# Kernel tuning notes

Hardware: AMD Instinct MI355X
Metric: run time of the kernel (lower is better)

The kernel has to match this reference:

```python
import jax, jax.numpy as jnp
import numpy as np

NEG_SLOPE = 0.2

def _lrelu(x):
    return jax.nn.leaky_relu(x, NEG_SLOPE)

def _seg_mean(vals, seg_ids, num_segments):
    # scatter-mean: sum per segment / count (count clamped to 1 -> zeros for empty nodes,
    # matching torch version where untouched nodes keep new_x == 0)
    s = jax.ops.segment_sum(vals, seg_ids, num_segments=num_segments)
    c = jax.ops.segment_sum(jnp.ones((vals.shape[0], 1), vals.dtype), seg_ids, num_segments=num_segments)
    return s / jnp.maximum(c, 1.0)

def _messages(x, src, dst, rel, ts, rel_emb, time_emb, W_rt, b_rt, W_fc, b_fc):
    # MessagePassing.forward: rel_e = lrelu(rel_t_trans(cat(rel_e, time_e)));
    # m = lrelu(fc(cat(x[src], rel_e, x[dst])))
    rel_e = _lrelu(jnp.concatenate([rel_emb[rel], time_emb[ts]], axis=-1) @ W_rt + b_rt)  # [E, 2h]
    m = _lrelu(jnp.concatenate([x[src], rel_e, x[dst]], axis=-1) @ W_fc + b_fc)           # [E, 2h]
    return m

def setup_inputs() -> dict:
    key = jax.random.key(0)
    ks = jax.random.split(key, 16)
    N, F, H, E, B = 20000, 128, 64, 200000, 256
    NUM_REL, NUM_TS, MAX_ENT = 200, 365, 5000
    s = 0.05
    inp = {}
    inp['x_feat'] = jax.random.normal(ks[0], (N, F), jnp.float32)
    inp['node_grp_emb'] = jax.random.normal(ks[1], (MAX_ENT, H), jnp.float32) * s
    inp['rel_emb'] = jax.random.normal(ks[2], (NUM_REL, H), jnp.float32) * s
    # TimeEncode (TGAT-style fixed frequencies): cos(t * 1/10^(linspace(0,9,H)))
    t = jnp.arange(NUM_TS, dtype=jnp.float32)
    freq = 1.0 / (10.0 ** jnp.linspace(0.0, 9.0, H, dtype=jnp.float32))
    inp['time_emb'] = jnp.cos(t[:, None] * freq[None, :])
    inp['W_node'] = jax.random.normal(ks[3], (F, H), jnp.float32) * s
    inp['b_node'] = jnp.zeros((H,), jnp.float32)
    inp['W_rt'] = jax.random.normal(ks[4], (2 * H, 2 * H), jnp.float32) * s
    inp['b_rt'] = jnp.zeros((2 * H,), jnp.float32)
    inp['W_fc'] = jax.random.normal(ks[5], (6 * H, 2 * H), jnp.float32) * s
    inp['b_fc'] = jnp.zeros((2 * H,), jnp.float32)
    inp['w_pred'] = jax.random.normal(ks[6], (6 * H, 1), jnp.float32) * s
    inp['b_pred'] = jnp.zeros((1,), jnp.float32)
    inp['node_ent'] = jax.random.randint(ks[7], (N,), 0, MAX_ENT)
    inp['edge_src'] = jax.random.randint(ks[8], (E,), 0, N)
    inp['edge_dst'] = jax.random.randint(ks[9], (E,), 0, N)
    inp['edge_type'] = jax.random.randint(ks[10], (E,), 0, NUM_REL)
    inp['edge_ts'] = jax.random.randint(ks[11], (E,), 0, NUM_TS)
    inp['q_s'] = jax.random.randint(ks[12], (B,), 0, N)
    inp['q_o'] = jax.random.randint(ks[13], (B,), 0, N)
    inp['q_r'] = jax.random.randint(ks[14], (B,), 0, NUM_REL)
    inp['q_t'] = jax.random.randint(ks[15], (B,), 0, NUM_TS)
    inp['num_hops'] = 2
    return inp

def reference(x_feat, node_grp_emb, rel_emb, time_emb, W_node, b_node, W_rt, b_rt,
              W_fc, b_fc, w_pred, b_pred, node_ent, edge_src, edge_dst, edge_type,
              edge_ts, q_s, q_o, q_r, q_t, num_hops):
    N = x_feat.shape[0]
    # node init: x = cat(lrelu(node_emb(feat)), node_grp_emb[ent])  (dropout = eval identity)
    x = jnp.concatenate([_lrelu(x_feat @ W_node + b_node), node_grp_emb[node_ent]], axis=-1)  # [N, 2h]
    # multi-hop gather -> edge MLP -> scatter-mean (frontier loop flattened to num_hops full passes)
    for _ in range(num_hops):
        m = _messages(x, edge_src, edge_dst, edge_type, edge_ts, rel_emb, time_emb, W_rt, b_rt, W_fc, b_fc)
        x = x + _seg_mean(m, edge_dst, N)
    # final aggregation only into query destination nodes q_o
    m = _messages(x, edge_src, edge_dst, edge_type, edge_ts, rel_emb, time_emb, W_rt, b_rt, W_fc, b_fc)
    agg = _seg_mean(m, edge_dst, N)
    qo_mask = jnp.zeros((N, 1), x.dtype).at[q_o].set(1.0)
    x = x + agg * qo_mask
    # query relation/time transform and prediction
    q_r_t = _lrelu(jnp.concatenate([rel_emb[q_r], time_emb[q_t]], axis=-1) @ W_rt + b_rt)  # [B, 2h]
    final_feat = jnp.concatenate([x[q_s], q_r_t, x[q_o]], axis=-1)                          # [B, 6h]
    out = jax.nn.sigmoid(final_feat @ w_pred + b_pred)
    return out.squeeze(-1)
```

## Files before the change

### kernel.cpp

```cpp
#include <hip/hip_runtime.h>
#include <cstddef>
#include <cstdint>

#define H 64
#define TWOH 128
#define CAP 96
#define LRELU(v) ((v) >= 0.f ? (v) : 0.2f * (v))

typedef __attribute__((ext_vector_type(4))) float f32x4;
typedef __attribute__((ext_vector_type(8))) short bf16x8;

__device__ inline unsigned short f2bf(float f) {
    union { float f; unsigned u; } v; v.f = f;
    unsigned u = v.u + 0x7FFFu + ((v.u >> 16) & 1u);
    return (unsigned short)(u >> 16);
}
__device__ inline float bf2f(unsigned u16) {
    union { unsigned u; float f; } v; v.u = u16 << 16; return v.f;
}

__global__ __launch_bounds__(256) void k_setup(
    const float* __restrict__ xf, const float* __restrict__ grp,
    const float* __restrict__ Wn, const float* __restrict__ bn,
    const int* __restrict__ ent, float* __restrict__ x, unsigned short* __restrict__ xb,
    const float* __restrict__ Wfc, unsigned short* __restrict__ WT,
    const float* __restrict__ rel_emb, const float* __restrict__ time_emb,
    const float* __restrict__ Wrt, const float* __restrict__ brt,
    const int* __restrict__ qr, const int* __restrict__ qt,
    float* __restrict__ AR, float* __restrict__ BT, float* __restrict__ qrt,
    const int* __restrict__ src, const int* __restrict__ dst,
    const int* __restrict__ etype, const int* __restrict__ ets,
    int* deg, int2* __restrict__ a_sc,
    int N, int E, int B, int NUM_REL, int NUM_TS,
    int NB_NI, int NB_TW, int NB_RT)
{
    int b = blockIdx.x, t = threadIdx.x;
    __shared__ float s_u[32][128];
    if (b < NB_NI) {
        int n0 = b * 32;
        int w = t >> 6, l = t & 63;
#pragma unroll
        for (int i = 0; i < 4; ++i) {
            int idx = t + i * 256; int r = idx >> 5, c4 = (idx & 31) * 4;
            int n = n0 + r;
            float4 v = make_float4(0.f, 0.f, 0.f, 0.f);
            if (n < N) v = *(const float4*)(xf + (size_t)n * 128 + c4);
            *(float4*)(&s_u[r][c4]) = v;
        }
        __syncthreads();
        float acc[8];
#pragma unroll
        for (int r = 0; r < 8; ++r) acc[r] = 0.f;
        for (int k = 0; k < 128; ++k) {
            float wv = Wn[k * H + l];
#pragma unroll
            for (int r = 0; r < 8; ++r) acc[r] += s_u[w * 8 + r][k] * wv;
        }
        float bb = bn[l];
        for (int r = 0; r < 8; ++r) {
            int n = n0 + w * 8 + r; if (n >= N) break;
            float v = LRELU(acc[r] + bb);
            float g = grp[(size_t)ent[n] * H + l];
            x[(size_t)n * TWOH + l]      = v;
            x[(size_t)n * TWOH + H + l]  = g;
            xb[(size_t)n * TWOH + l]     = f2bf(v);
            xb[(size_t)n * TWOH + H + l] = f2bf(g);
        }
    } else if (b < NB_NI + NB_TW) {
        int tid = (b - NB_NI) * 256 + t;
        int m = tid >> 14, rem = tid & 16383, col = rem >> 7, k = rem & 127;
        WT[(size_t)m * 16384 + col * 128 + k] = f2bf(Wfc[((size_t)m * 128 + k) * 128 + col]);
    } else if (b < NB_NI + NB_TW + NB_RT) {
        int sub = t >> 7, tt = t & 127;
        int row = (b - NB_NI - NB_TW) * 2 + sub;
        int RT_ROWS = NUM_REL + NUM_TS + B;
        int valid = row < RT_ROWS;
        int type = 0, ridx = 0;
        if (valid) {
            if (row < NUM_REL)               { type = 0; ridx = row; }
            else if (row < NUM_REL + NUM_TS) { type = 1; ridx = row - NUM_REL; }
            else                             { type = 2; ridx = row - NUM_REL - NUM_TS; }
        }
        float lv = 0.f;
        if (valid) {
            if (type == 0)      lv = (tt < H) ? rel_emb[(size_t)ridx * H + tt] : 0.f;
            else if (type == 1) lv = (tt >= H) ? time_emb[(size_t)ridx * H + (tt - H)] : 0.f;
            else                lv = (tt < H) ? rel_emb[(size_t)qr[ridx] * H + tt]
                                              : time_emb[(size_t)qt[ridx] * H + (tt - H)];
        }
        s_u[sub][tt] = lv;
        __syncthreads();
        if (valid) {
            float acc = 0.f;
            for (int k = 0; k < 128; ++k) acc += s_u[sub][k] * Wrt[(size_t)k * TWOH + tt];
            if (type != 1) acc += brt[tt];
            if (type == 2) acc = LRELU(acc);
            if (type == 0)      AR[(size_t)ridx * TWOH + tt]  = acc;
            else if (type == 1) BT[(size_t)ridx * TWOH + tt]  = acc;
            else                qrt[(size_t)ridx * TWOH + tt] = acc;
        }
    } else {
        int e = (b - NB_NI - NB_TW - NB_RT) * 256 + t;
        if (e < E) {
            int dn = dst[e];
            int pos = atomicAdd(&deg[dn], 1);
            a_sc[(size_t)dn * CAP + pos] = make_int2(src[e], etype[e] * NUM_TS + ets[e]);
        }
    }
}

__global__ __launch_bounds__(256) void k_mid3(
    const float* __restrict__ AR, const float* __restrict__ BT,
    const unsigned short* __restrict__ WT, const float* __restrict__ bd,
    unsigned short* __restrict__ RE2b, int NC, int NUM_TS,
    const unsigned short* __restrict__ xb,
    unsigned short* __restrict__ XSb, unsigned short* __restrict__ XDb, int N,
    const int* __restrict__ qo, int* maski, int* __restrict__ qlist, int* cntQ, int B,
    int NB_RE2, int NB_G)
{
    __shared__ __align__(16) char smem[33280];
    int b = blockIdx.x, t = threadIdx.x;
    if (b < NB_RE2) {
        unsigned short* s_mid = (unsigned short*)smem;
        unsigned short* s_out = (unsigned short*)(smem + 16384);
        int* s_rel = (int*)(smem + 32768);
        int* s_ts  = s_rel + 64;
        const unsigned short* WTr = WT + 16384;
        int c0 = b * 64;
        if (t < 64) {
            int cc = c0 + t; if (cc >= NC) cc = NC - 1;
            int rel = cc / NUM_TS;
            s_rel[t] = rel; s_ts[t] = cc - rel * NUM_TS;
        }
        __syncthreads();
#pragma unroll
        for (int i = 0; i < 4; ++i) {
            int idx = t + i * 256;
            int r = idx >> 4, c8 = (idx & 15) * 8;
            const float* ar = AR + (size_t)s_rel[r] * TWOH + c8;
            const float* bt = BT + (size_t)s_ts[r]  * TWOH + c8;
            unsigned short tmp[8] __attribute__((aligned(16)));
#pragma unroll
            for (int j = 0; j < 8; ++j) {
                float v = ar[j] + bt[j];
                tmp[j] = f2bf(LRELU(v));
            }
            int byte = r * 256 + ((c8 * 2) ^ ((r & 7) << 4));
            *(bf16x8*)(smem + byte) = *(bf16x8*)tmp;
        }
        __syncthreads();
        int w = t >> 6, l = t & 63;
        int arow = w * 16 + (l & 15);
        int kgrp = (l >> 4) * 8;
        f32x4 acc[8];
#pragma unroll
        for (int ct = 0; ct < 8; ++ct) acc[ct] = (f32x4){0.f, 0.f, 0.f, 0.f};
#pragma unroll
        for (int kc = 0; kc < 128; kc += 32) {
            int kb = (kc + kgrp) * 2;
            bf16x8 a = *(bf16x8*)((char*)s_mid + arow * 256 + (kb ^ ((arow & 7) << 4)));
#pragma unroll
            for (int ct = 0; ct < 8; ++ct) {
                bf16x8 bb = *(const bf16x8*)(WTr + (size_t)(ct * 16 + (l & 15)) * TWOH + kc + kgrp);
                acc[ct] = __builtin_amdgcn_mfma_f32_16x16x32_bf16(a, bb, acc[ct], 0, 0, 0);
            }
        }
#pragma unroll
        for (int ct = 0; ct < 8; ++ct) {
#pragma unroll
            for (int reg = 0; reg < 4; ++reg) {
                int row  = w * 16 + (l >> 4) * 4 + reg;
                int colb = (ct * 16 + (l & 15)) * 2;
                *(unsigned short*)((char*)s_out + row * 256 + (colb ^ ((row & 7) << 4)))
                    = f2bf(acc[ct][reg]);
            }
        }
        __syncthreads();
#pragma unroll
        for (int i = 0; i < 4; ++i) {
            int idx = t + i * 256;
            int r = idx >> 4, c16 = (idx & 15) * 16;
            int cc = c0 + r;
            if (cc >= NC) continue;
            bf16x8 v = *(bf16x8*)((char*)s_out + r * 256 + (c16 ^ ((r & 7) << 4)));
            *(bf16x8*)(RE2b + (size_t)cc * TWOH + c16 / 2) = v;
        }
    } else if (b < NB_RE2 + NB_G) {
        unsigned short* s_oS = (unsigned short*)smem;
        unsigned short* s_oD = (unsigned short*)(smem + 8192);
        int bid = b - NB_RE2;
        int n0 = (bid >> 1) * 64;
        int colbase = (bid & 1) * 64;
        const unsigned short* WTs = WT;
        const unsigned short* WTd = WT + 32768;
        int w = t >> 6, l = t & 63;
        int node = n0 + w * 16 + (l & 15); if (node >= N) node = N - 1;
        int kgrp = (l >> 4) * 8;
        f32x4 aS[4], aD[4];
#pragma unroll
        for (int ct = 0; ct < 4; ++ct) { aS[ct] = (f32x4){0.f,0.f,0.f,0.f}; aD[ct] = (f32x4){0.f,0.f,0.f,0.f}; }
#pragma unroll
        for (int kc = 0; kc < 128; kc += 32) {
            bf16x8 a = *(const bf16x8*)(xb + (size_t)node * TWOH + kc + kgrp);
#pragma unroll
            for (int ct = 0; ct < 4; ++ct) {
                size_t wo = (size_t)(colbase + ct * 16 + (l & 15)) * TWOH + kc + kgrp;
                bf16x8 b1 = *(const bf16x8*)(WTs + wo);
                bf16x8 b2 = *(const bf16x8*)(WTd + wo);
                aS[ct] = __builtin_amdgcn_mfma_f32_16x16x32_bf16(a, b1, aS[ct], 0, 0, 0);
                aD[ct] = __builtin_amdgcn_mfma_f32_16x16x32_bf16(a, b2, aD[ct], 0, 0, 0);
            }
        }
#pragma unroll
        for (int ct = 0; ct < 4; ++ct) {
            int lc = ct * 16 + (l & 15);
            float bb = bd[colbase + lc];
#pragma unroll
            for (int reg = 0; reg < 4; ++reg) {
                int row = w * 16 + (l >> 4) * 4 + reg;
                int off = row * 128 + ((lc * 2) ^ ((row & 7) << 4));
                *(unsigned short*)((char*)s_oS + off) = f2bf(aS[ct][reg]);
                *(unsigned short*)((char*)s_oD + off) = f2bf(aD[ct][reg] + bb);
            }
        }
        __syncthreads();
#pragma unroll
        for (int i = 0; i < 2; ++i) {
            int idx = t + i * 256;
            int r = idx >> 3, c16 = (idx & 7) * 16;
            int n = n0 + r; if (n >= N) continue;
            int off = r * 128 + (c16 ^ ((r & 7) << 4));
            *(bf16x8*)(XSb + (size_t)n * TWOH + colbase + c16 / 2) = *(bf16x8*)((char*)s_oS + off);
            *(bf16x8*)(XDb + (size_t)n * TWOH + colbase + c16 / 2) = *(bf16x8*)((char*)s_oD + off);
        }
    } else {
        for (int i = t; i < B; i += 256) {
            int n = qo[i];
            if (atomicExch(&maski[n], 1) == 0) qlist[atomicAdd(cntQ, 1)] = n;
        }
    }
}

__global__ __launch_bounds__(256) void k_gemm_dual_mfma(
    const unsigned short* __restrict__ xb,
    const unsigned short* __restrict__ WTs, const unsigned short* __restrict__ WTd,
    const float* __restrict__ bd,
    unsigned short* __restrict__ XSb, unsigned short* __restrict__ XDb, int M)
{
    __shared__ unsigned short s_oS[64 * 64];
    __shared__ unsigned short s_oD[64 * 64];
    int t  = threadIdx.x;
    int n0 = blockIdx.x * 64;
    int colbase = blockIdx.y * 64;
    int w = t >> 6, l = t & 63;
    int node = n0 + w * 16 + (l & 15); if (node >= M) node = M - 1;
    int kgrp = (l >> 4) * 8;
    f32x4 aS[4], aD[4];
#pragma unroll
    for (int ct = 0; ct < 4; ++ct) { aS[ct] = (f32x4){0.f,0.f,0.f,0.f}; aD[ct] = (f32x4){0.f,0.f,0.f,0.f}; }
#pragma unroll
    for (int kc = 0; kc < 128; kc += 32) {
        bf16x8 a = *(const bf16x8*)(xb + (size_t)node * TWOH + kc + kgrp);
#pragma unroll
        for (int ct = 0; ct < 4; ++ct) {
            size_t wo = (size_t)(colbase + ct * 16 + (l & 15)) * TWOH + kc + kgrp;
            bf16x8 b1 = *(const bf16x8*)(WTs + wo);
            bf16x8 b2 = *(const bf16x8*)(WTd + wo);
            aS[ct] = __builtin_amdgcn_mfma_f32_16x16x32_bf16(a, b1, aS[ct], 0, 0, 0);
            aD[ct] = __builtin_amdgcn_mfma_f32_16x16x32_bf16(a, b2, aD[ct], 0, 0, 0);
        }
    }
#pragma unroll
    for (int ct = 0; ct < 4; ++ct) {
        int lc = ct * 16 + (l & 15);
        float bb = bd[colbase + lc];
#pragma unroll
        for (int reg = 0; reg < 4; ++reg) {
            int row = w * 16 + (l >> 4) * 4 + reg;
            int off = row * 128 + ((lc * 2) ^ ((row & 7) << 4));
            *(unsigned short*)((char*)s_oS + off) = f2bf(aS[ct][reg]);
            *(unsigned short*)((char*)s_oD + off) = f2bf(aD[ct][reg] + bb);
        }
    }
    __syncthreads();
#pragma unroll
    for (int i = 0; i < 2; ++i) {
        int idx = t + i * 256;
        int r = idx >> 3, c16 = (idx & 7) * 16;
        int n = n0 + r; if (n >= M) continue;
        int off = r * 128 + (c16 ^ ((r & 7) << 4));
        *(bf16x8*)(XSb + (size_t)n * TWOH + colbase + c16 / 2) = *(bf16x8*)((char*)s_oS + off);
        *(bf16x8*)(XDb + (size_t)n * TWOH + colbase + c16 / 2) = *(bf16x8*)((char*)s_oD + off);
    }
}

__global__ __launch_bounds__(256) void k_gemm_list(
    const unsigned short* __restrict__ xb, const unsigned short* __restrict__ WT,
    const float* __restrict__ bd,
    const int* __restrict__ listS, const int* __restrict__ cntS,
    const int* __restrict__ qlist, const int* __restrict__ cntQ,
    unsigned short* __restrict__ XSb, unsigned short* __restrict__ XDb)
{
    int mode = blockIdx.y;
    const int* list = mode ? qlist : listS;
    int c = mode ? *cntQ : *cntS;
    int r0 = blockIdx.x * 64;
    if (r0 >= c) return;
    const unsigned short* W = mode ? (WT + 32768) : WT;
    unsigned short* Out = mode ? XDb : XSb;

    __shared__ unsigned short s_out[64 * 128];
    int t = threadIdx.x;
    int w = t >> 6, l = t & 63;
    int slot = r0 + w * 16 + (l & 15); if (slot >= c) slot = c - 1;
    int node = list[slot];
    int kgrp = (l >> 4) * 8;
    f32x4 acc[8];
#pragma unroll
    for (int ct = 0; ct < 8; ++ct) acc[ct] = (f32x4){0.f, 0.f, 0.f, 0.f};
#pragma unroll
    for (int kc = 0; kc < 128; kc += 32) {
        bf16x8 a = *(const bf16x8*)(xb + (size_t)node * TWOH + kc + kgrp);
#pragma unroll
        for (int ct = 0; ct < 8; ++ct) {
            bf16x8 b = *(const bf16x8*)(W + (size_t)(ct * 16 + (l & 15)) * TWOH + kc + kgrp);
            acc[ct] = __builtin_amdgcn_mfma_f32_16x16x32_bf16(a, b, acc[ct], 0, 0, 0);
        }
    }
#pragma unroll
    for (int ct = 0; ct < 8; ++ct) {
        int col = ct * 16 + (l & 15);
        float bb = mode ? bd[col] : 0.f;
#pragma unroll
        for (int reg = 0; reg < 4; ++reg) {
            int row = w * 16 + (l >> 4) * 4 + reg;
            int off = row * 256 + ((col * 2) ^ ((row & 7) << 4));
            *(unsigned short*)((char*)s_out + off) = f2bf(acc[ct][reg] + bb);
        }
    }
    __syncthreads();
#pragma unroll
    for (int i = 0; i < 4; ++i) {
        int idx = t + i * 256;
        int r = idx >> 4, c16 = (idx & 15) * 16;
        if (r0 + r >= c) continue;
        int n = list[r0 + r];
        bf16x8 v = *(bf16x8*)((char*)s_out + r * 256 + (c16 ^ ((r & 7) << 4)));
        *(bf16x8*)(Out + (size_t)n * TWOH + c16 / 2) = v;
    }
}

__global__ __launch_bounds__(256) void k_agg(
    float* __restrict__ x, unsigned short* __restrict__ xb,
    const unsigned short* __restrict__ XSb, const unsigned short* __restrict__ XDb,
    const unsigned short* __restrict__ RE2b,
    const int* __restrict__ deg, const int2* __restrict__ a_sc,
    const int* __restrict__ list, const int* __restrict__ cnt, int N,
    int nAggBlk, const int* __restrict__ qlistM, const int* __restrict__ cntQM,
    int* maskS, int* __restrict__ listS, int* cntS)
{
    if ((int)blockIdx.x >= nAggBlk) {
        int slot = ((int)blockIdx.x - nAggBlk) * 4 + (threadIdx.x >> 6);
        if (slot >= *cntQM) return;
        int n = qlistM[slot];
        int lane = threadIdx.x & 63;
        int start = n * CAP, end = start + deg[n];
        for (int p = start + lane; p < end; p += 64) {
            int s = a_sc[p].x;
            if (atomicExch(&maskS[s], 1) == 0) listS[atomicAdd(cntS, 1)] = s;
        }
        return;
    }
    int slot = blockIdx.x * 4 + (threadIdx.x >> 6);
    int n;
    if (list) {
        if (slot >= *cnt) return;
        n = list[slot];
    } else {
        n = slot; if (n >= N) return;
    }
    int lane = threadIdx.x & 63;
    int half = lane >> 5;
    int c4   = (lane & 31) * 4;
    int d    = deg[n];
    int start = n * CAP, end = start + d;
    uint2 cvu = *(const uint2*)(XDb + (size_t)n * TWOH + c4);
    float cv0 = bf2f(cvu.x & 0xFFFFu), cv1 = bf2f(cvu.x >> 16);
    float cv2 = bf2f(cvu.y & 0xFFFFu), cv3 = bf2f(cvu.y >> 16);
    float a0 = 0.f, a1 = 0.f, a2 = 0.f, a3 = 0.f;
    for (int base = start; base < end; base += 64) {
        int m = end - base; if (m > 64) m = 64;
        int2 my = make_int2(0, 0);
        if (base + lane < end) my = a_sc[base + lane];
        int j = 0;
        for (; j + 4 <= m; j += 4) {
            int iA = j + half, iB = j + 2 + half;
            int sA = __shfl(my.x, iA), cA = __shfl(my.y, iA);
            int sB = __shfl(my.x, iB), cB = __shfl(my.y, iB);
            uint2 uA = *(const uint2*)(XSb  + (size_t)sA * TWOH + c4);
            uint2 vA = *(const uint2*)(RE2b + (size_t)cA * TWOH + c4);
            uint2 uB = *(const uint2*)(XSb  + (size_t)sB * TWOH + c4);
            uint2 vB = *(const uint2*)(RE2b + (size_t)cB * TWOH + c4);
            float p0 = bf2f(uA.x & 0xFFFFu) + bf2f(vA.x & 0xFFFFu) + cv0; p0 = LRELU(p0);
            float p1 = bf2f(uA.x >> 16)     + bf2f(vA.x >> 16)     + cv1; p1 = LRELU(p1);
            float p2 = bf2f(uA.y & 0xFFFFu) + bf2f(vA.y & 0xFFFFu) + cv2; p2 = LRELU(p2);
            float p3 = bf2f(uA.y >> 16)     + bf2f(vA.y >> 16)     + cv3; p3 = LRELU(p3);
            float q0 = bf2f(uB.x & 0xFFFFu) + bf2f(vB.x & 0xFFFFu) + cv0; q0 = LRELU(q0);
            float q1 = bf2f(uB.x >> 16)     + bf2f(vB.x >> 16)     + cv1; q1 = LRELU(q1);
            float q2 = bf2f(uB.y & 0xFFFFu) + bf2f(vB.y & 0xFFFFu) + cv2; q2 = LRELU(q2);
            float q3 = bf2f(uB.y >> 16)     + bf2f(vB.y >> 16)     + cv3; q3 = LRELU(q3);
            a0 += p0 + q0; a1 += p1 + q1; a2 += p2 + q2; a3 += p3 + q3;
        }
        for (; j < m; j += 2) {
            int iA = j + half;
            int sA = __shfl(my.x, iA), cA = __shfl(my.y, iA);
            if (iA < m) {
                uint2 uA = *(const uint2*)(XSb  + (size_t)sA * TWOH + c4);
                uint2 vA = *(const uint2*)(RE2b + (size_t)cA * TWOH + c4);
                float p0 = bf2f(uA.x & 0xFFFFu) + bf2f(vA.x & 0xFFFFu) + cv0; p0 = LRELU(p0);
                float p1 = bf2f(uA.x >> 16)     + bf2f(vA.x >> 16)     + cv1; p1 = LRELU(p1);
                float p2 = bf2f(uA.y & 0xFFFFu) + bf2f(vA.y & 0xFFFFu) + cv2; p2 = LRELU(p2);
                float p3 = bf2f(uA.y >> 16)     + bf2f(vA.y >> 16)     + cv3; p3 = LRELU(p3);
                a0 += p0; a1 += p1; a2 += p2; a3 += p3;
            }
        }
    }
    a0 += __shfl_xor(a0, 32); a1 += __shfl_xor(a1, 32);
    a2 += __shfl_xor(a2, 32); a3 += __shfl_xor(a3, 32);
    if (half == 0) {
        float inv = 1.f / (float)(d > 1 ? d : 1);
        float* xr = x + (size_t)n * TWOH + c4;
        float4 xv = *(float4*)xr;
        xv.x += a0 * inv; xv.y += a1 * inv; xv.z += a2 * inv; xv.w += a3 * inv;
        *(float4*)xr = xv;
        uint2 xbv;
        xbv.x = ((unsigned)f2bf(xv.y) << 16) | f2bf(xv.x);
        xbv.y = ((unsigned)f2bf(xv.w) << 16) | f2bf(xv.z);
        *(uint2*)(xb + (size_t)n * TWOH + c4) = xbv;
    }
}

__global__ __launch_bounds__(64) void k_predict(
    const float* __restrict__ x, const float* __restrict__ qrt,
    const float* __restrict__ wp, const float* __restrict__ bp,
    const int* __restrict__ qs, const int* __restrict__ qo,
    float* __restrict__ out, int B)
{
    int b = blockIdx.x;
    if (b >= B) return;
    int lane = threadIdx.x;
    const float* fs = x + (size_t)qs[b] * TWOH;
    const float* fo = x + (size_t)qo[b] * TWOH;
    const float* fr = qrt + (size_t)b * TWOH;
    float acc = 0.f;
#pragma unroll
    for (int i = 0; i < 2; ++i) {
        int k = lane + i * 64;
        acc += fs[k] * wp[k] + fr[k] * wp[128 + k] + fo[k] * wp[256 + k];
    }
#pragma unroll
    for (int o = 32; o > 0; o >>= 1) acc += __shfl_down(acc, o);
    if (lane == 0) out[b] = 1.f / (1.f + expf(-(acc + bp[0])));
}

extern "C" void kernel_launch(void* const* d_in, const int* in_sizes, int n_in,
                              void* d_out, int out_size, void* d_ws, size_t ws_size,
                              hipStream_t stream)
{
    const float* x_feat   = (const float*)d_in[0];
    const float* grp      = (const float*)d_in[1];
    const float* rel_emb  = (const float*)d_in[2];
    const float* time_emb = (const float*)d_in[3];
    const float* W_node   = (const float*)d_in[4];
    const float* b_node   = (const float*)d_in[5];
    const float* W_rt     = (const float*)d_in[6];
    const float* b_rt     = (const float*)d_in[7];
    const float* W_fc     = (const float*)d_in[8];
    const float* b_fc     = (const float*)d_in[9];
    const float* w_pred   = (const float*)d_in[10];
    const float* b_pred   = (const float*)d_in[11];
    const int* node_ent   = (const int*)d_in[12];
    const int* edge_src   = (const int*)d_in[13];
    const int* edge_dst   = (const int*)d_in[14];
    const int* edge_type  = (const int*)d_in[15];
    const int* edge_ts    = (const int*)d_in[16];
    const int* q_s        = (const int*)d_in[17];
    const int* q_o        = (const int*)d_in[18];
    const int* q_r        = (const int*)d_in[19];
    const int* q_t        = (const int*)d_in[20];
    const int NUM_HOPS = 2;

    int N       = in_sizes[12];
    int E       = in_sizes[13];
    int B       = in_sizes[17];
    int NUM_TS  = in_sizes[3] / H;
    int NUM_REL = in_sizes[2] / H;
    int NC      = NUM_REL * NUM_TS;

    char* ws = (char*)d_ws;
    size_t off = 0;
    auto alloc = [&](size_t bytes) {
        void* p = ws + off; off += (bytes + 255) & ~(size_t)255; return p;
    };
    float*          x    = (float*)         alloc((size_t)N * TWOH * 4);
    unsigned short* xb   = (unsigned short*)alloc((size_t)N * TWOH * 2);
    unsigned short* RE2b = (unsigned short*)alloc((size_t)NC * TWOH * 2);
    unsigned short* XSb  = (unsigned short*)alloc((size_t)N * TWOH * 2);
    unsigned short* XDb  = (unsigned short*)alloc((size_t)N * TWOH * 2);
    unsigned short* WT   = (unsigned short*)alloc((size_t)3 * 128 * 128 * 2);
    float* AR   = (float*)alloc((size_t)NUM_REL * TWOH * 4);
    float* BT   = (float*)alloc((size_t)NUM_TS  * TWOH * 4);
    float* qrt  = (float*)alloc((size_t)B * TWOH * 4);
    int*   degi  = (int*)alloc((size_t)N * 4);
    int*   maski = (int*)alloc((size_t)N * 4);
    int*   maskS = (int*)alloc((size_t)N * 4);
    int*   cnts  = (int*)alloc(256);
    int*   qlist = (int*)alloc((size_t)B * 4);
    int*   listS = (int*)alloc((size_t)N * 4);
    int2*  a_sc  = (int2*)alloc((size_t)N * CAP * 8);
    (void)ws_size; (void)n_in; (void)out_size;
    int* cntQ = cnts, * cntS = cnts + 1;

    hipMemsetAsync(degi, 0, (size_t)((char*)cnts + 256 - (char*)degi), stream);

    int NB_NI  = (N + 31) / 32;
    int NB_TW  = 192;
    int NB_RT  = (NUM_REL + NUM_TS + B + 1) / 2;
    int NB_SC  = (E + 255) / 256;
    int NB_RE2 = (NC + 63) / 64;
    int NB_G   = ((N + 63) / 64) * 2;
    int NB_AGG = (N + 3) / 4;
    int NB_MS  = (B + 3) / 4;

    k_setup<<<NB_NI + NB_TW + NB_RT + NB_SC, 256, 0, stream>>>(
        x_feat, grp, W_node, b_node, node_ent, x, xb,
        W_fc, WT, rel_emb, time_emb, W_rt, b_rt, q_r, q_t, AR, BT, qrt,
        edge_src, edge_dst, edge_type, edge_ts, degi, a_sc,
        N, E, B, NUM_REL, NUM_TS, NB_NI, NB_TW, NB_RT);
    k_mid3<<<NB_RE2 + NB_G + 1, 256, 0, stream>>>(
        AR, BT, WT, b_fc, RE2b, NC, NUM_TS, xb, XSb, XDb, N,
        q_o, maski, qlist, cntQ, B, NB_RE2, NB_G);

    k_agg<<<NB_AGG + NB_MS, 256, 0, stream>>>(
        x, xb, XSb, XDb, RE2b, degi, a_sc, nullptr, nullptr, N,
        NB_AGG, qlist, cntQ, maskS, listS, cntS);
    for (int pass = 1; pass < NUM_HOPS; ++pass) {
        dim3 grid((N + 63) / 64, 2);
        k_gemm_dual_mfma<<<grid, 256, 0, stream>>>(
            xb, WT, WT + 32768, b_fc, XSb, XDb, N);
        k_agg<<<NB_AGG, 256, 0, stream>>>(
            x, xb, XSb, XDb, RE2b, degi, a_sc, nullptr, nullptr, N,
            NB_AGG, qlist, cntQ, maskS, listS, cntS);
    }
    {
        dim3 grid((N + 63) / 64, 2);
        k_gemm_list<<<grid, 256, 0, stream>>>(xb, WT, b_fc, listS, cntS, qlist, cntQ,
                                              XSb, XDb);
    }
    k_agg<<<NB_MS, 256, 0, stream>>>(
        x, xb, XSb, XDb, RE2b, degi, a_sc, qlist, cntQ, N,
        NB_MS, qlist, cntQ, maskS, listS, cntS);

    k_predict<<<B, 64, 0, stream>>>(x, qrt, w_pred, b_pred, q_s, q_o, (float*)d_out, B);
}
```

Measured before the change: 152.8 us.

## Rebalance setup kernels and replace memset with in-kernel zeroing

Drops the hipMemsetAsync and zeroes the degree, mask and counter buffers inside the first kernel. Node init and edge scatter move into the second kernel alongside the RE2 precompute. The first-hop GEMM and the query-source marking go into a new third kernel, which lets k_agg lose its extra branch. This removes one launch/memset, rebalances the blocks across the setup stages and simplifies the aggregation kernel, at the cost of one more kernel boundary in the setup chain.

```diff
diff --git a/kernel.cpp b/kernel.cpp
--- a/kernel.cpp
+++ b/kernel.cpp
@@ -19,60 +19,27 @@
     union { unsigned u; float f; } v; v.u = u16 << 16; return v.f;
 }
 
-__global__ __launch_bounds__(256) void k_setup(
-    const float* __restrict__ xf, const float* __restrict__ grp,
-    const float* __restrict__ Wn, const float* __restrict__ bn,
-    const int* __restrict__ ent, float* __restrict__ x, unsigned short* __restrict__ xb,
+__global__ __launch_bounds__(256) void k_pre(
+    int* __restrict__ zb, int nz,
     const float* __restrict__ Wfc, unsigned short* __restrict__ WT,
     const float* __restrict__ rel_emb, const float* __restrict__ time_emb,
     const float* __restrict__ Wrt, const float* __restrict__ brt,
     const int* __restrict__ qr, const int* __restrict__ qt,
     float* __restrict__ AR, float* __restrict__ BT, float* __restrict__ qrt,
-    const int* __restrict__ src, const int* __restrict__ dst,
-    const int* __restrict__ etype, const int* __restrict__ ets,
-    int* deg, int2* __restrict__ a_sc,
-    int N, int E, int B, int NUM_REL, int NUM_TS,
-    int NB_NI, int NB_TW, int NB_RT)
+    int NUM_REL, int NUM_TS, int B, int NB_Z, int NB_TW)
 {
     int b = blockIdx.x, t = threadIdx.x;
-    __shared__ float s_u[32][128];
-    if (b < NB_NI) {
-        int n0 = b * 32;
-        int w = t >> 6, l = t & 63;
-#pragma unroll
-        for (int i = 0; i < 4; ++i) {
-            int idx = t + i * 256; int r = idx >> 5, c4 = (idx & 31) * 4;
-            int n = n0 + r;
-            float4 v = make_float4(0.f, 0.f, 0.f, 0.f);
-            if (n < N) v = *(const float4*)(xf + (size_t)n * 128 + c4);
-            *(float4*)(&s_u[r][c4]) = v;
-        }
-        __syncthreads();
-        float acc[8];
-#pragma unroll
-        for (int r = 0; r < 8; ++r) acc[r] = 0.f;
-        for (int k = 0; k < 128; ++k) {
-            float wv = Wn[k * H + l];
-#pragma unroll
-            for (int r = 0; r < 8; ++r) acc[r] += s_u[w * 8 + r][k] * wv;
-        }
-        float bb = bn[l];
-        for (int r = 0; r < 8; ++r) {
-            int n = n0 + w * 8 + r; if (n >= N) break;
-            float v = LRELU(acc[r] + bb);
-            float g = grp[(size_t)ent[n] * H + l];
-            x[(size_t)n * TWOH + l]      = v;
-            x[(size_t)n * TWOH + H + l]  = g;
-            xb[(size_t)n * TWOH + l]     = f2bf(v);
-            xb[(size_t)n * TWOH + H + l] = f2bf(g);
-        }
-    } else if (b < NB_NI + NB_TW) {
-        int tid = (b - NB_NI) * 256 + t;
+    if (b < NB_Z) {
+        int i = b * 256 + t;
+        if (i < nz) zb[i] = 0;
+    } else if (b < NB_Z + NB_TW) {
+        int tid = (b - NB_Z) * 256 + t;
         int m = tid >> 14, rem = tid & 16383, col = rem >> 7, k = rem & 127;
         WT[(size_t)m * 16384 + col * 128 + k] = f2bf(Wfc[((size_t)m * 128 + k) * 128 + col]);
-    } else if (b < NB_NI + NB_TW + NB_RT) {
+    } else {
+        __shared__ float s_u[2][128];
         int sub = t >> 7, tt = t & 127;
-        int row = (b - NB_NI - NB_TW) * 2 + sub;
+        int row = (b - NB_Z - NB_TW) * 2 + sub;
         int RT_ROWS = NUM_REL + NUM_TS + B;
         int valid = row < RT_ROWS;
         int type = 0, ridx = 0;
@@ -99,24 +66,22 @@
             else if (type == 1) BT[(size_t)ridx * TWOH + tt]  = acc;
             else                qrt[(size_t)ridx * TWOH + tt] = acc;
         }
-    } else {
-        int e = (b - NB_NI - NB_TW - NB_RT) * 256 + t;
-        if (e < E) {
-            int dn = dst[e];
-            int pos = atomicAdd(&deg[dn], 1);
-            a_sc[(size_t)dn * CAP + pos] = make_int2(src[e], etype[e] * NUM_TS + ets[e]);
-        }
-    }
-}
-
-__global__ __launch_bounds__(256) void k_mid3(
+    }
+}
+
+__global__ __launch_bounds__(256) void k_setup2(
     const float* __restrict__ AR, const float* __restrict__ BT,
-    const unsigned short* __restrict__ WT, const float* __restrict__ bd,
+    const unsigned short* __restrict__ WT,
     unsigned short* __restrict__ RE2b, int NC, int NUM_TS,
-    const unsigned short* __restrict__ xb,
-    unsigned short* __restrict__ XSb, unsigned short* __restrict__ XDb, int N,
+    const float* __restrict__ xf, const float* __restrict__ grp,
+    const float* __restrict__ Wn, const float* __restrict__ bn,
+    const int* __restrict__ ent, float* __restrict__ x, unsigned short* __restrict__ xb,
+    int N,
+    const int* __restrict__ src, const int* __restrict__ dst,
+    const int* __restrict__ etype, const int* __restrict__ ets,
+    int* deg, int2* __restrict__ a_sc, int E,
     const int* __restrict__ qo, int* maski, int* __restrict__ qlist, int* cntQ, int B,
-    int NB_RE2, int NB_G)
+    int NB_RE2, int NB_NI, int NB_SC)
 {
     __shared__ __align__(16) char smem[33280];
     int b = blockIdx.x, t = threadIdx.x;
@@ -185,12 +150,66 @@
             bf16x8 v = *(bf16x8*)((char*)s_out + r * 256 + (c16 ^ ((r & 7) << 4)));
             *(bf16x8*)(RE2b + (size_t)cc * TWOH + c16 / 2) = v;
         }
-    } else if (b < NB_RE2 + NB_G) {
-        unsigned short* s_oS = (unsigned short*)smem;
-        unsigned short* s_oD = (unsigned short*)(smem + 8192);
-        int bid = b - NB_RE2;
-        int n0 = (bid >> 1) * 64;
-        int colbase = (bid & 1) * 64;
+    } else if (b < NB_RE2 + NB_NI) {
+        float (*s_u)[128] = (float(*)[128])smem;
+        int n0 = (b - NB_RE2) * 32;
+        int w = t >> 6, l = t & 63;
+#pragma unroll
+        for (int i = 0; i < 4; ++i) {
+            int idx = t + i * 256; int r = idx >> 5, c4 = (idx & 31) * 4;
+            int n = n0 + r;
+            float4 v = make_float4(0.f, 0.f, 0.f, 0.f);
+            if (n < N) v = *(const float4*)(xf + (size_t)n * 128 + c4);
+            *(float4*)(&s_u[r][c4]) = v;
+        }
+        __syncthreads();
+        float acc[8];
+#pragma unroll
+        for (int r = 0; r < 8; ++r) acc[r] = 0.f;
+        for (int k = 0; k < 128; ++k) {
+            float wv = Wn[k * H + l];
+#pragma unroll
+            for (int r = 0; r < 8; ++r) acc[r] += s_u[w * 8 + r][k] * wv;
+        }
+        float bb = bn[l];
+        for (int r = 0; r < 8; ++r) {
+            int n = n0 + w * 8 + r; if (n >= N) break;
+            float v = LRELU(acc[r] + bb);
+            float g = grp[(size_t)ent[n] * H + l];
+            x[(size_t)n * TWOH + l]      = v;
+            x[(size_t)n * TWOH + H + l]  = g;
+            xb[(size_t)n * TWOH + l]     = f2bf(v);
+            xb[(size_t)n * TWOH + H + l] = f2bf(g);
+        }
+    } else if (b < NB_RE2 + NB_NI + NB_SC) {
+        int e = (b - NB_RE2 - NB_NI) * 256 + t;
+        if (e < E) {
+            int dn = dst[e];
+            int pos = atomicAdd(&deg[dn], 1);
+            a_sc[(size_t)dn * CAP + pos] = make_int2(src[e], etype[e] * NUM_TS + ets[e]);
+        }
+    } else {
+        for (int i = t; i < B; i += 256) {
+            int n = qo[i];
+            if (atomicExch(&maski[n], 1) == 0) qlist[atomicAdd(cntQ, 1)] = n;
+        }
+    }
+}
+
+__global__ __launch_bounds__(256) void k_g0m(
+    const unsigned short* __restrict__ xb, const unsigned short* __restrict__ WT,
+    const float* __restrict__ bd,
+    unsigned short* __restrict__ XSb, unsigned short* __restrict__ XDb, int N,
+    const int* __restrict__ qlist, const int* __restrict__ cntQ,
+    const int* __restrict__ deg, const int2* __restrict__ a_sc,
+    int* maskS, int* __restrict__ listS, int* cntS, int NB_G)
+{
+    __shared__ unsigned short s_oS[64 * 64];
+    __shared__ unsigned short s_oD[64 * 64];
+    int b = blockIdx.x, t = threadIdx.x;
+    if (b < NB_G) {
+        int n0 = (b >> 1) * 64;
+        int colbase = (b & 1) * 64;
         const unsigned short* WTs = WT;
         const unsigned short* WTd = WT + 32768;
         int w = t >> 6, l = t & 63;
@@ -234,9 +253,14 @@
             *(bf16x8*)(XDb + (size_t)n * TWOH + colbase + c16 / 2) = *(bf16x8*)((char*)s_oD + off);
         }
     } else {
-        for (int i = t; i < B; i += 256) {
-            int n = qo[i];
-            if (atomicExch(&maski[n], 1) == 0) qlist[atomicAdd(cntQ, 1)] = n;
+        int slot = (b - NB_G) * 4 + (t >> 6);
+        if (slot >= *cntQ) return;
+        int n = qlist[slot];
+        int lane = t & 63;
+        int start = n * CAP, end = start + deg[n];
+        for (int p = start + lane; p < end; p += 64) {
+            int s = a_sc[p].x;
+            if (atomicExch(&maskS[s], 1) == 0) listS[atomicAdd(cntS, 1)] = s;
         }
     }
 }
@@ -355,22 +379,8 @@
     const unsigned short* __restrict__ XSb, const unsigned short* __restrict__ XDb,
     const unsigned short* __restrict__ RE2b,
     const int* __restrict__ deg, const int2* __restrict__ a_sc,
-    const int* __restrict__ list, const int* __restrict__ cnt, int N,
-    int nAggBlk, const int* __restrict__ qlistM, const int* __restrict__ cntQM,
-    int* maskS, int* __restrict__ listS, int* cntS)
-{
-    if ((int)blockIdx.x >= nAggBlk) {
-        int slot = ((int)blockIdx.x - nAggBlk) * 4 + (threadIdx.x >> 6);
-        if (slot >= *cntQM) return;
-        int n = qlistM[slot];
-        int lane = threadIdx.x & 63;
-        int start = n * CAP, end = start + deg[n];
-        for (int p = start + lane; p < end; p += 64) {
-            int s = a_sc[p].x;
-            if (atomicExch(&maskS[s], 1) == 0) listS[atomicAdd(cntS, 1)] = s;
-        }
-        return;
-    }
+    const int* __restrict__ list, const int* __restrict__ cnt, int N)
+{
     int slot = blockIdx.x * 4 + (threadIdx.x >> 6);
     int n;
     if (list) {
@@ -511,55 +521,56 @@
     float* AR   = (float*)alloc((size_t)NUM_REL * TWOH * 4);
     float* BT   = (float*)alloc((size_t)NUM_TS  * TWOH * 4);
     float* qrt  = (float*)alloc((size_t)B * TWOH * 4);
-    int*   degi  = (int*)alloc((size_t)N * 4);
-    int*   maski = (int*)alloc((size_t)N * 4);
-    int*   maskS = (int*)alloc((size_t)N * 4);
-    int*   cnts  = (int*)alloc(256);
-    int*   qlist = (int*)alloc((size_t)B * 4);
-    int*   listS = (int*)alloc((size_t)N * 4);
-    int2*  a_sc  = (int2*)alloc((size_t)N * CAP * 8);
+    int nz = 3 * N + 64;
+    int*  zb    = (int*)alloc((size_t)nz * 4);
+    int*  degi  = zb;
+    int*  maski = zb + N;
+    int*  maskS = zb + 2 * N;
+    int*  cnts  = zb + 3 * N;
+    int*  qlist = (int*)alloc((size_t)B * 4);
+    int*  listS = (int*)alloc((size_t)N * 4);
+    int2* a_sc  = (int2*)alloc((size_t)N * CAP * 8);
     (void)ws_size; (void)n_in; (void)out_size;
     int* cntQ = cnts, * cntS = cnts + 1;
 
-    hipMemsetAsync(degi, 0, (size_t)((char*)cnts + 256 - (char*)degi), stream);
-
-    int NB_NI  = (N + 31) / 32;
+    int NB_Z   = (nz + 255) / 256;
     int NB_TW  = 192;
     int NB_RT  = (NUM_REL + NUM_TS + B + 1) / 2;
+    int NB_NI  = (N + 31) / 32;
     int NB_SC  = (E + 255) / 256;
     int NB_RE2 = (NC + 63) / 64;
     int NB_G   = ((N + 63) / 64) * 2;
     int NB_AGG = (N + 3) / 4;
     int NB_MS  = (B + 3) / 4;
 
-    k_setup<<<NB_NI + NB_TW + NB_RT + NB_SC, 256, 0, stream>>>(
-        x_feat, grp, W_node, b_node, node_ent, x, xb,
-        W_fc, WT, rel_emb, time_emb, W_rt, b_rt, q_r, q_t, AR, BT, qrt,
-        edge_src, edge_dst, edge_type, edge_ts, degi, a_sc,
-        N, E, B, NUM_REL, NUM_TS, NB_NI, NB_TW, NB_RT);
-    k_mid3<<<NB_RE2 + NB_G + 1, 256, 0, stream>>>(
-        AR, BT, WT, b_fc, RE2b, NC, NUM_TS, xb, XSb, XDb, N,
-        q_o, maski, qlist, cntQ, B, NB_RE2, NB_G);
-
-    k_agg<<<NB_AGG + NB_MS, 256, 0, stream>>>(
-        x, xb, XSb, XDb, RE2b, degi, a_sc, nullptr, nullptr, N,
-        NB_AGG, qlist, cntQ, maskS, listS, cntS);
+    k_pre<<<NB_Z + NB_TW + NB_RT, 256, 0, stream>>>(
+        zb, nz, W_fc, WT, rel_emb, time_emb, W_rt, b_rt, q_r, q_t,
+        AR, BT, qrt, NUM_REL, NUM_TS, B, NB_Z, NB_TW);
+    k_setup2<<<NB_RE2 + NB_NI + NB_SC + 1, 256, 0, stream>>>(
+        AR, BT, WT, RE2b, NC, NUM_TS,
+        x_feat, grp, W_node, b_node, node_ent, x, xb, N,
+        edge_src, edge_dst, edge_type, edge_ts, degi, a_sc, E,
+        q_o, maski, qlist, cntQ, B, NB_RE2, NB_NI, NB_SC);
+    k_g0m<<<NB_G + NB_MS, 256, 0, stream>>>(
+        xb, WT, b_fc, XSb, XDb, N, qlist, cntQ, degi, a_sc,
+        maskS, listS, cntS, NB_G);
+
+    k_agg<<<NB_AGG, 256, 0, stream>>>(x, xb, XSb, XDb, RE2b, degi, a_sc,
+                                      nullptr, nullptr, N);
     for (int pass = 1; pass < NUM_HOPS; ++pass) {
         dim3 grid((N + 63) / 64, 2);
         k_gemm_dual_mfma<<<grid, 256, 0, stream>>>(
             xb, WT, WT + 32768, b_fc, XSb, XDb, N);
-        k_agg<<<NB_AGG, 256, 0, stream>>>(
-            x, xb, XSb, XDb, RE2b, degi, a_sc, nullptr, nullptr, N,
-            NB_AGG, qlist, cntQ, maskS, listS, cntS);
+        k_agg<<<NB_AGG, 256, 0, stream>>>(x, xb, XSb, XDb, RE2b, degi, a_sc,
+                                          nullptr, nullptr, N);
     }
     {
         dim3 grid((N + 63) / 64, 2);
         k_gemm_list<<<grid, 256, 0, stream>>>(xb, WT, b_fc, listS, cntS, qlist, cntQ,
                                               XSb, XDb);
     }
-    k_agg<<<NB_MS, 256, 0, stream>>>(
-        x, xb, XSb, XDb, RE2b, degi, a_sc, qlist, cntQ, N,
-        NB_MS, qlist, cntQ, maskS, listS, cntS);
+    k_agg<<<NB_MS, 256, 0, stream>>>(x, xb, XSb, XDb, RE2b, degi, a_sc,
+                                     qlist, cntQ, N);
 
     k_predict<<<B, 64, 0, stream>>>(x, qrt, w_pred, b_pred, q_s, q_o, (float*)d_out, B);
 }
```

New measurement: 146.2 us. 1.05x faster.
